# Performance work log

Measured on AMD Instinct MI355X. Metric: run time of the kernel, lower is better.

The kernel has to match this reference:

```python
import math
import jax, jax.numpy as jnp
import numpy as np

HIDDEN = 2880
HEAD_DIM = 64
N_HEADS = 64
N_KV = 8
Q_MULT = N_HEADS // N_KV  # 8
QKV_DIM = HEAD_DIM * (N_HEADS + 2 * N_KV)  # 5120
SLIDING_WINDOW = 128
SM_SCALE = 1.0 / math.sqrt(HEAD_DIM)
ROPE_BASE = 150000.0
ROPE_SCALING = 32.0
INIT_CTX = 4096
NTK_ALPHA = 1.0
NTK_BETA = 32.0
EPS = 1e-5
N_TOKENS = 1536


def rope_tables(n):
    # YaRN-style inv_freq mixing (scaling_factor > 1 branch)
    d = HEAD_DIM
    freq = ROPE_BASE ** (jnp.arange(0, d, 2, dtype=jnp.float32) / d)
    concentration = 0.1 * math.log(ROPE_SCALING) + 1.0
    d_half = d / 2
    low = d_half * math.log(INIT_CTX / (NTK_BETA * 2 * math.pi)) / math.log(ROPE_BASE)
    high = d_half * math.log(INIT_CTX / (NTK_ALPHA * 2 * math.pi)) / math.log(ROPE_BASE)
    interpolation = 1.0 / (ROPE_SCALING * freq)
    extrapolation = 1.0 / freq
    ramp = (jnp.arange(d_half, dtype=jnp.float32) - low) / (high - low)
    mask = 1.0 - jnp.clip(ramp, 0.0, 1.0)
    inv_freq = interpolation * (1.0 - mask) + extrapolation * mask
    t = jnp.arange(n, dtype=jnp.float32)
    freqs = t[:, None] * inv_freq[None, :]  # (n, d/2)
    return jnp.cos(freqs) * concentration, jnp.sin(freqs) * concentration


def apply_rotary(x, cos, sin):
    # x: (n, H, d); cos/sin: (n, d/2)
    c = cos[:, None, :]
    s = sin[:, None, :]
    x1, x2 = jnp.split(x, 2, axis=-1)
    return jnp.concatenate([x1 * c - x2 * s, x2 * c + x1 * s], axis=-1)


def setup_inputs() -> dict:
    key = jax.random.key(0)
    ks = jax.random.split(key, 7)
    x = jax.random.normal(ks[0], (N_TOKENS, HIDDEN), dtype=jnp.float32)
    norm_scale = jnp.ones((HIDDEN,), dtype=jnp.float32)
    qkv_w = jax.random.normal(ks[1], (QKV_DIM, HIDDEN), dtype=jnp.float32) * 0.02
    qkv_b = jax.random.normal(ks[2], (QKV_DIM,), dtype=jnp.float32) * 0.02
    out_w = jax.random.normal(ks[3], (HIDDEN, HEAD_DIM * N_HEADS), dtype=jnp.float32) * 0.02
    out_b = jax.random.normal(ks[4], (HIDDEN,), dtype=jnp.float32) * 0.02
    sinks = jax.random.normal(ks[5], (N_HEADS,), dtype=jnp.float32)
    return {"x": x, "norm_scale": norm_scale, "qkv_w": qkv_w, "qkv_b": qkv_b,
            "out_w": out_w, "out_b": out_b, "sinks": sinks}


def reference(x, norm_scale, qkv_w, qkv_b, out_w, out_b, sinks):
    n = x.shape[0]
    # RMSNorm (fp32)
    t = x * jax.lax.rsqrt(jnp.mean(x * x, axis=-1, keepdims=True) + EPS) * norm_scale
    # fused QKV projection
    qkv = t @ qkv_w.T + qkv_b  # (n, QKV_DIM)
    q = qkv[:, : N_HEADS * HEAD_DIM].reshape(n, N_KV, Q_MULT, HEAD_DIM)
    k = qkv[:, N_HEADS * HEAD_DIM : (N_HEADS + N_KV) * HEAD_DIM].reshape(n, N_KV, HEAD_DIM)
    v = qkv[:, (N_HEADS + N_KV) * HEAD_DIM :].reshape(n, N_KV, HEAD_DIM)
    # RoPE
    cos, sin = rope_tables(n)
    q = apply_rotary(q.reshape(n, N_HEADS, HEAD_DIM), cos, sin).reshape(n, N_KV, Q_MULT, HEAD_DIM)
    k = apply_rotary(k, cos, sin)
    # attention with causal + sliding-window mask and sink logits
    i = jnp.arange(n)[:, None]
    j = jnp.arange(n)[None, :]
    allowed = (j <= i) & (j > i - SLIDING_WINDOW)
    mask = jnp.where(allowed, 0.0, -jnp.inf).astype(jnp.float32)  # (q, k)
    scores = jnp.einsum('qhmd,khd->hmqk', q, k) * SM_SCALE + mask[None, None, :, :]
    s = sinks.reshape(N_KV, Q_MULT, 1, 1)
    s = jnp.broadcast_to(s, (N_KV, Q_MULT, n, 1))
    logits = jnp.concatenate([scores, s], axis=-1)
    w = jax.nn.softmax(logits, axis=-1)[..., :-1]  # drop sink column
    attn = jnp.einsum('hmqk,khd->qhmd', w, v).reshape(n, N_HEADS * HEAD_DIM)
    # output projection + residual
    return x + attn @ out_w.T + out_b
```

## Files before the change

### kernel.cpp

```cpp
#include <hip/hip_runtime.h>

typedef __attribute__((ext_vector_type(8))) short bf16x8;
typedef __attribute__((ext_vector_type(4))) float f32x4;

#define HIDDEN 2880
#define QKV_DIM 5120
#define NH 64
#define NKV 8
#define HD 64
#define ATT_DIM 4096
#define WINDOW 128
#define SM_SCALE 0.125f

__device__ __forceinline__ ushort f2bf(float f) {
  union { float f; unsigned u; } a; a.f = f;
  unsigned r = a.u + 0x7fffu + ((a.u >> 16) & 1u);
  return (ushort)(r >> 16);
}

__device__ __forceinline__ void gload_lds16(const void* g, void* l) {
  __builtin_amdgcn_global_load_lds((const __attribute__((address_space(1))) void*)g,
                                   (__attribute__((address_space(3))) void*)l, 16, 0, 0);
}

__global__ __launch_bounds__(256) void cvt_f32_bf16(const float* __restrict__ in,
                                                    ushort* __restrict__ out, int n4) {
  int i = blockIdx.x * blockDim.x + threadIdx.x;
  int stride = gridDim.x * blockDim.x;
  for (; i < n4; i += stride) {
    float4 v = ((const float4*)in)[i];
    ushort4 o = { f2bf(v.x), f2bf(v.y), f2bf(v.z), f2bf(v.w) };
    ((ushort4*)out)[i] = o;
  }
}

__global__ __launch_bounds__(256) void rmsnorm_bf16(const float* __restrict__ x,
                                                    const float* __restrict__ scale,
                                                    ushort* __restrict__ t) {
  int row = blockIdx.x;
  int tid = threadIdx.x;
  const float4* xr = (const float4*)(x + (size_t)row * HIDDEN);
  float4 a0 = xr[tid];
  float4 a1 = xr[tid + 256];
  bool has2 = tid < 208;
  float4 a2 = has2 ? xr[tid + 512] : float4{0.f, 0.f, 0.f, 0.f};
  float ss = a0.x*a0.x + a0.y*a0.y + a0.z*a0.z + a0.w*a0.w
           + a1.x*a1.x + a1.y*a1.y + a1.z*a1.z + a1.w*a1.w
           + a2.x*a2.x + a2.y*a2.y + a2.z*a2.z + a2.w*a2.w;
  for (int m = 1; m < 64; m <<= 1) ss += __shfl_xor(ss, m, 64);
  __shared__ float red[4];
  if ((tid & 63) == 0) red[tid >> 6] = ss;
  __syncthreads();
  ss = red[0] + red[1] + red[2] + red[3];
  float r = rsqrtf(ss / (float)HIDDEN + 1e-5f);
  ushort4* tr = (ushort4*)(t + (size_t)row * HIDDEN);
  const float4* sc4 = (const float4*)scale;
  {
    float4 s = sc4[tid];
    ushort4 o = { f2bf(a0.x*r*s.x), f2bf(a0.y*r*s.y), f2bf(a0.z*r*s.z), f2bf(a0.w*r*s.w) };
    tr[tid] = o;
  }
  {
    float4 s = sc4[tid + 256];
    ushort4 o = { f2bf(a1.x*r*s.x), f2bf(a1.y*r*s.y), f2bf(a1.z*r*s.z), f2bf(a1.w*r*s.w) };
    tr[tid + 256] = o;
  }
  if (has2) {
    float4 s = sc4[tid + 512];
    ushort4 o = { f2bf(a2.x*r*s.x), f2bf(a2.y*r*s.y), f2bf(a2.z*r*s.z), f2bf(a2.w*r*s.w) };
    tr[tid + 512] = o;
  }
}

template <int MASK_N>
__global__ __launch_bounds__(512)
void gemm_8p(const ushort* __restrict__ A, const ushort* __restrict__ B,
             float* __restrict__ P, int M, int N, int K, int NSK) {
  __shared__ __align__(16) ushort Al[2][256 * 64];
  __shared__ __align__(16) ushort Bl[2][256 * 64];
  const int tid = threadIdx.x;
  const int wave = tid >> 6, lane = tid & 63;
  const int l15 = lane & 15, hi = lane >> 4;

  int nwg = gridDim.x, orig = blockIdx.x;
  int q8 = nwg >> 3, r8 = nwg & 7, xcd = orig & 7, seq = orig >> 3;
  int swz = (xcd < r8 ? xcd * (q8 + 1) : r8 * (q8 + 1) + (xcd - r8) * q8) + seq;
  int nm = M >> 8;
  int bm = swz % nm, bn = swz / nm;
  const int row0 = bm * 256, col0 = bn * 256;
  const int sk = blockIdx.y;
  const int NTtot = K >> 6;
  const int tt0 = sk * NTtot / NSK, tt1 = (sk + 1) * NTtot / NSK;
  float* Pp = P + (size_t)sk * M * N;

  const int wrow = (wave >> 2) * 128;
  const int wcol = (wave & 3) * 64;
  const int srow = lane >> 3;
  const int schunk = (lane & 7) ^ srow;

  f32x4 acc[8][4] = {};

  auto stageA = [&](int t, int r) {
    int row = row0 + r * 64 + wave * 8 + srow;
    gload_lds16(A + (size_t)row * K + (t << 6) + schunk * 8,
                &Al[t & 1][(r * 64 + wave * 8) * 64]);
  };
  auto stageB = [&](int t, int r) {
    int brow = col0 + r * 64 + wave * 8 + srow;
    if (MASK_N) { if (brow > N - 1) brow = N - 1; }
    gload_lds16(B + (size_t)brow * K + (t << 6) + schunk * 8,
                &Bl[t & 1][(r * 64 + wave * 8) * 64]);
  };
  auto stageAll = [&](int t) {
#pragma unroll
    for (int r = 0; r < 4; ++r) { stageA(t, r); stageB(t, r); }
  };
  auto LDA = [&](bf16x8 (&dst)[4][2], int mh, const char* base) {
#pragma unroll
    for (int mt = 0; mt < 4; ++mt)
#pragma unroll
      for (int ks = 0; ks < 2; ++ks) {
        int rr = wrow + mh * 64 + mt * 16 + l15;
        int off = (rr * 128 + ks * 64 + hi * 16) ^ ((rr & 7) << 4);
        dst[mt][ks] = *(const bf16x8*)(base + off);
      }
  };
  auto LDB = [&](bf16x8 (&dst)[2][2], int nh, const char* base) {
#pragma unroll
    for (int nt = 0; nt < 2; ++nt)
#pragma unroll
      for (int ks = 0; ks < 2; ++ks) {
        int rr = wcol + nh * 32 + nt * 16 + l15;
        int off = (rr * 128 + ks * 64 + hi * 16) ^ ((rr & 7) << 4);
        dst[nt][ks] = *(const bf16x8*)(base + off);
      }
  };
  auto MMA = [&](bf16x8 (&a)[4][2], bf16x8 (&b)[2][2], int mh, int nh) {
    __builtin_amdgcn_s_setprio(1);
#pragma unroll
    for (int ks = 0; ks < 2; ++ks)
#pragma unroll
      for (int nt = 0; nt < 2; ++nt)
#pragma unroll
        for (int mt = 0; mt < 4; ++mt)
          acc[mh * 4 + mt][nh * 2 + nt] = __builtin_amdgcn_mfma_f32_16x16x32_bf16(
              a[mt][ks], b[nt][ks], acc[mh * 4 + mt][nh * 2 + nt], 0, 0, 0);
    __builtin_amdgcn_s_setprio(0);
  };

  stageAll(tt0);
  bool two = (tt1 - tt0 > 1);
  if (two) {
    stageAll(tt0 + 1);
    asm volatile("s_waitcnt vmcnt(8)" ::: "memory");
  } else {
    asm volatile("s_waitcnt vmcnt(0)" ::: "memory");
  }
  __builtin_amdgcn_s_barrier();

  for (int t = tt0; t < tt1; ++t) {
    const char* Ab = (const char*)&Al[t & 1][0];
    const char* Bb = (const char*)&Bl[t & 1][0];
    bool pre = (t + 2 < tt1);
    bf16x8 afr[4][2], bf0[2][2], bf1[2][2];
    LDA(afr, 0, Ab);
    LDB(bf0, 0, Bb);
    __builtin_amdgcn_s_barrier();
    MMA(afr, bf0, 0, 0);
    __builtin_amdgcn_s_barrier();
    LDB(bf1, 1, Bb);
    if (pre) { stageA(t + 2, 0); stageA(t + 2, 2); }
    __builtin_amdgcn_s_barrier();
    MMA(afr, bf1, 0, 1);
    __builtin_amdgcn_s_barrier();
    LDA(afr, 1, Ab);
    if (pre) { stageB(t + 2, 0); stageB(t + 2, 1); stageB(t + 2, 2); stageB(t + 2, 3); }
    __builtin_amdgcn_s_barrier();
    MMA(afr, bf1, 1, 1);
    __builtin_amdgcn_s_barrier();
    if (pre) { stageA(t + 2, 1); stageA(t + 2, 3); }
    __builtin_amdgcn_s_barrier();
    MMA(afr, bf0, 1, 0);
    if (pre) asm volatile("s_waitcnt vmcnt(8)" ::: "memory");
    else     asm volatile("s_waitcnt vmcnt(0)" ::: "memory");
    __builtin_amdgcn_s_barrier();
  }

#pragma unroll
  for (int mtg = 0; mtg < 8; ++mtg) {
#pragma unroll
    for (int nt = 0; nt < 4; ++nt) {
#pragma unroll
      for (int rr = 0; rr < 4; ++rr) {
        int row = row0 + wrow + mtg * 16 + (hi << 2) + rr;
        int col = col0 + wcol + nt * 16 + l15;
        if (!MASK_N || col < N) Pp[(size_t)row * N + col] = acc[mtg][nt][rr];
      }
    }
  }
}

__global__ __launch_bounds__(256)
void reduce_out(const float* __restrict__ x, const float* __restrict__ b,
                const float* __restrict__ p, int nsk, size_t stride,
                float* __restrict__ out, int n4, int N) {
  int i = blockIdx.x * blockDim.x + threadIdx.x;
  if (i >= n4) return;
  float4 v = ((const float4*)x)[i];
  int col = (i * 4) % N;
  float4 bb = *(const float4*)(b + col);
  v.x += bb.x; v.y += bb.y; v.z += bb.z; v.w += bb.w;
  for (int s = 0; s < nsk; ++s) {
    float4 pv = *(const float4*)(p + s * stride + (size_t)i * 4);
    v.x += pv.x; v.y += pv.y; v.z += pv.z; v.w += pv.w;
  }
  ((float4*)out)[i] = v;
}

__global__ __launch_bounds__(256)
void rope_split(const float* __restrict__ p, size_t stride, const float* __restrict__ qkvb,
                ushort* __restrict__ qb, ushort* __restrict__ kb, ushort* __restrict__ vb) {
  int tok = blockIdx.x;
  int tid = threadIdx.x;
  __shared__ float cs[32], sn[32];
  if (tid < 32) {
    float d = (float)tid;
    float freq = powf(150000.0f, d / 32.0f);
    float conc = 0.1f * logf(32.0f) + 1.0f;
    float lg = logf(150000.0f);
    float low = 32.0f * logf(4096.0f / (32.0f * 6.2831853f)) / lg;
    float high = 32.0f * logf(4096.0f / 6.2831853f) / lg;
    float ramp = (d - low) / (high - low);
    float cl = fminf(fmaxf(ramp, 0.0f), 1.0f);
    float mask = 1.0f - cl;
    float inv_freq = (1.0f - mask) / (32.0f * freq) + mask / freq;
    float fr = (float)tok * inv_freq;
    cs[tid] = cosf(fr) * conc;
    sn[tid] = sinf(fr) * conc;
  }
  __syncthreads();
  const float* r0 = p + (size_t)tok * QKV_DIM;
  const float* r1 = r0 + stride;
  auto ld = [&](int c) { return r0[c] + r1[c] + qkvb[c]; };
#pragma unroll
  for (int it = 0; it < 8; ++it) {
    int pp = tid + it * 256;
    int hd = pp >> 5, d = pp & 31;
    float x1 = ld(hd * 64 + d), x2 = ld(hd * 64 + d + 32);
    float c = cs[d], s = sn[d];
    size_t o = ((size_t)tok * NH + hd) * HD + d;
    qb[o] = f2bf(x1 * c - x2 * s);
    qb[o + 32] = f2bf(x2 * c + x1 * s);
  }
  {
    int pp = tid;
    int hd = pp >> 5, d = pp & 31;
    float x1 = ld(4096 + hd * 64 + d), x2 = ld(4096 + hd * 64 + d + 32);
    float c = cs[d], s = sn[d];
    size_t o = ((size_t)tok * NKV + hd) * HD + d;
    kb[o] = f2bf(x1 * c - x2 * s);
    kb[o + 32] = f2bf(x2 * c + x1 * s);
  }
#pragma unroll
  for (int it = 0; it < 2; ++it) {
    int pp = tid + it * 256;
    vb[(size_t)tok * (NKV * HD) + pp] = f2bf(ld(4608 + pp));
  }
}

__global__ __launch_bounds__(512)
void attn_fused(const ushort* __restrict__ qb, const ushort* __restrict__ kb,
                const ushort* __restrict__ vb, const float* __restrict__ sinks,
                ushort* __restrict__ attn, int n) {
  __shared__ __align__(16) ushort Kl[160 * 64];
  __shared__ __align__(16) ushort Vt[64 * 168];
  __shared__ __align__(16) ushort Pl[8][16 * 40];
  int tid = threadIdx.x;
  int wave = tid >> 6, lane = tid & 63;
  int l15 = lane & 15, hi = lane >> 4;
  int qstart = blockIdx.x * 16;
  int kv = blockIdx.y;
  int head = kv * 8 + wave;
  int key0 = qstart - 128;

  for (int i = 0; i < 3; ++i) {
    int rowb = i * 64 + wave * 8;
    if (rowb < 160) {
      int r = rowb + (lane >> 3);
      int gj = key0 + r; if (gj < 0) gj = 0;
      int chunk = (lane & 7) ^ (lane >> 3);
      gload_lds16(kb + ((size_t)gj * NKV + kv) * HD + chunk * 8, Kl + rowb * 64);
    }
  }
  for (int e = tid; e < 160 * 16; e += 512) {
    int j = e >> 4, d4 = (e & 15) << 2;
    int gj = key0 + j; if (gj < 0) gj = 0;
    ushort4 v = *(const ushort4*)(vb + ((size_t)gj * NKV + kv) * HD + d4);
    Vt[(d4 + 0) * 168 + j] = v.x;
    Vt[(d4 + 1) * 168 + j] = v.y;
    Vt[(d4 + 2) * 168 + j] = v.z;
    Vt[(d4 + 3) * 168 + j] = v.w;
  }
  bf16x8 qf[2];
#pragma unroll
  for (int ks = 0; ks < 2; ++ks) {
    int r = qstart + l15;
    int kk = ks * 32 + hi * 8;
    qf[ks] = *(const bf16x8*)(qb + ((size_t)r * NH + head) * HD + kk);
  }
  __syncthreads();

  f32x4 s[10] = {};
#pragma unroll
  for (int nt = 0; nt < 10; ++nt) {
#pragma unroll
    for (int ks = 0; ks < 2; ++ks) {
      int r = nt * 16 + l15;
      int off = (r * 128 + (ks * 32 + hi * 8) * 2) ^ ((r & 7) << 4);
      bf16x8 kf = *(const bf16x8*)((const char*)Kl + off);
      s[nt] = __builtin_amdgcn_mfma_f32_16x16x32_bf16(qf[ks], kf, s[nt], 0, 0, 0);
    }
  }

  float lrow[4];
  float snk = sinks[head];
#pragma unroll
  for (int r = 0; r < 4; ++r) {
    int i = qstart + hi * 4 + r;
    float mx = -1e30f;
#pragma unroll
    for (int nt = 0; nt < 10; ++nt) {
      int j = key0 + nt * 16 + l15;
      bool ok = (j >= 0) && (j <= i) && (j > i - WINDOW);
      float val = ok ? s[nt][r] * SM_SCALE : -1e30f;
      s[nt][r] = val;
      mx = fmaxf(mx, val);
    }
    mx = fmaxf(mx, __shfl_xor(mx, 1, 64));
    mx = fmaxf(mx, __shfl_xor(mx, 2, 64));
    mx = fmaxf(mx, __shfl_xor(mx, 4, 64));
    mx = fmaxf(mx, __shfl_xor(mx, 8, 64));
    mx = fmaxf(mx, snk);
    float sum = 0.f;
#pragma unroll
    for (int nt = 0; nt < 10; ++nt) {
      float pv = __expf(s[nt][r] - mx);
      s[nt][r] = pv;
      sum += pv;
    }
    sum += __shfl_xor(sum, 1, 64);
    sum += __shfl_xor(sum, 2, 64);
    sum += __shfl_xor(sum, 4, 64);
    sum += __shfl_xor(sum, 8, 64);
    sum += __expf(snk - mx);
    lrow[r] = sum;
  }

  f32x4 o[4] = {};
#pragma unroll
  for (int kc = 0; kc < 5; ++kc) {
#pragma unroll
    for (int t2 = 0; t2 < 2; ++t2) {
      int nt = kc * 2 + t2;
#pragma unroll
      for (int r = 0; r < 4; ++r)
        Pl[wave][(hi * 4 + r) * 40 + t2 * 16 + l15] = f2bf(s[nt][r]);
    }
    bf16x8 pa = *(const bf16x8*)(&Pl[wave][l15 * 40 + hi * 8]);
#pragma unroll
    for (int nt = 0; nt < 4; ++nt) {
      int d = nt * 16 + l15;
      int kk = kc * 32 + hi * 8;
      bf16x8 vf = *(const bf16x8*)(&Vt[d * 168 + kk]);
      o[nt] = __builtin_amdgcn_mfma_f32_16x16x32_bf16(pa, vf, o[nt], 0, 0, 0);
    }
  }

#pragma unroll
  for (int nt = 0; nt < 4; ++nt)
#pragma unroll
    for (int r = 0; r < 4; ++r) {
      int row = qstart + hi * 4 + r;
      int d = nt * 16 + l15;
      float val = o[nt][r] / lrow[r];
      attn[((size_t)row * NH + head) * HD + d] = f2bf(val);
    }
}

extern "C" void kernel_launch(void* const* d_in, const int* in_sizes, int n_in,
                              void* d_out, int out_size, void* d_ws, size_t ws_size,
                              hipStream_t stream) {
  const float* x      = (const float*)d_in[0];
  const float* nscale = (const float*)d_in[1];
  const float* qkv_w  = (const float*)d_in[2];
  const float* qkv_b  = (const float*)d_in[3];
  const float* out_w  = (const float*)d_in[4];
  const float* out_b  = (const float*)d_in[5];
  const float* sinks  = (const float*)d_in[6];
  float* out = (float*)d_out;
  int n = in_sizes[0] / HIDDEN;

  char* ws = (char*)d_ws;
  size_t off = 0;
  auto alloc = [&](size_t bytes) {
    char* p = ws + off;
    off += (bytes + 255) & ~(size_t)255;
    return p;
  };
  ushort* t_bf    = (ushort*)alloc((size_t)n * HIDDEN * 2);
  ushort* qkvw_bf = (ushort*)alloc((size_t)QKV_DIM * HIDDEN * 2);
  ushort* outw_bf = (ushort*)alloc((size_t)HIDDEN * ATT_DIM * 2);
  ushort* q_bf    = (ushort*)alloc((size_t)n * NH * HD * 2);
  ushort* k_bf    = (ushort*)alloc((size_t)n * NKV * HD * 2);
  ushort* v_bf    = (ushort*)alloc((size_t)n * NKV * HD * 2);
  ushort* attn    = (ushort*)alloc((size_t)n * ATT_DIM * 2);
  size_t qkv_ps = (size_t)n * QKV_DIM;
  size_t out_ps = (size_t)n * HIDDEN;
  size_t pelems = 2 * qkv_ps > 3 * out_ps ? 2 * qkv_ps : 3 * out_ps;
  float* partials = (float*)alloc(pelems * 4);

  cvt_f32_bf16<<<2048, 256, 0, stream>>>(qkv_w, qkvw_bf, QKV_DIM * HIDDEN / 4);
  cvt_f32_bf16<<<2048, 256, 0, stream>>>(out_w, outw_bf, HIDDEN * ATT_DIM / 4);
  rmsnorm_bf16<<<n, 256, 0, stream>>>(x, nscale, t_bf);
  gemm_8p<0><<<dim3((n / 256) * (QKV_DIM / 256), 2), 512, 0, stream>>>(
      t_bf, qkvw_bf, partials, n, QKV_DIM, HIDDEN, 2);
  rope_split<<<n, 256, 0, stream>>>(partials, qkv_ps, qkv_b, q_bf, k_bf, v_bf);
  attn_fused<<<dim3(n / 16, NKV), 512, 0, stream>>>(q_bf, k_bf, v_bf, sinks, attn, n);
  gemm_8p<1><<<dim3((n / 256) * 12, 3), 512, 0, stream>>>(
      attn, outw_bf, partials, n, HIDDEN, ATT_DIM, 3);
  reduce_out<<<(n * HIDDEN / 4 + 255) / 256, 256, 0, stream>>>(
      x, out_b, partials, 3, out_ps, out, n * HIDDEN / 4, HIDDEN);
}
```

Measured before the change: 180.6 us.

## Replace split-K 256x256 GEMMs with smaller-tile triple-buffered GEMMs and fused epilogue

Replaces the split-K 256x256 GEMM with a 128xBROWS tile GEMM that uses a three-stage LDS ring buffer and no split-K. The QKV GEMM now writes its result once and the RoPE kernel reads a single buffer. The output projection uses 128x192 tiles, which cover HIDDEN exactly and remove the N masking, and adds bias and residual in its epilogue, so the reduce kernel is gone. This drops the partial-sum writes and reads and one kernel launch. In exchange each block does a longer K loop with a smaller tile, which changes arithmetic intensity and occupancy.

```diff
diff --git a/kernel.cpp b/kernel.cpp
--- a/kernel.cpp
+++ b/kernel.cpp
@@ -72,12 +72,14 @@
   }
 }
 
-template <int MASK_N>
+template <int NFRAG, int EPI>
 __global__ __launch_bounds__(512)
-void gemm_8p(const ushort* __restrict__ A, const ushort* __restrict__ B,
-             float* __restrict__ P, int M, int N, int K, int NSK) {
-  __shared__ __align__(16) ushort Al[2][256 * 64];
-  __shared__ __align__(16) ushort Bl[2][256 * 64];
+void gemm_3b(const ushort* __restrict__ A, const ushort* __restrict__ B,
+             const float* __restrict__ bias, const float* __restrict__ resid,
+             float* __restrict__ C, int M, int N, int K) {
+  constexpr int BROWS = 64 * NFRAG;
+  __shared__ __align__(16) ushort Al[3][128 * 64];
+  __shared__ __align__(16) ushort Bl[3][BROWS * 64];
   const int tid = threadIdx.x;
   const int wave = tid >> 6, lane = tid & 63;
   const int l15 = lane & 15, hi = lane >> 4;
@@ -85,140 +87,108 @@
   int nwg = gridDim.x, orig = blockIdx.x;
   int q8 = nwg >> 3, r8 = nwg & 7, xcd = orig & 7, seq = orig >> 3;
   int swz = (xcd < r8 ? xcd * (q8 + 1) : r8 * (q8 + 1) + (xcd - r8) * q8) + seq;
-  int nm = M >> 8;
+  int nm = M >> 7;
   int bm = swz % nm, bn = swz / nm;
-  const int row0 = bm * 256, col0 = bn * 256;
-  const int sk = blockIdx.y;
-  const int NTtot = K >> 6;
-  const int tt0 = sk * NTtot / NSK, tt1 = (sk + 1) * NTtot / NSK;
-  float* Pp = P + (size_t)sk * M * N;
-
-  const int wrow = (wave >> 2) * 128;
-  const int wcol = (wave & 3) * 64;
+  const int row0 = bm * 128, col0 = bn * BROWS;
+  const int wrow = (wave >> 2) * 64;
+  const int wcol = (wave & 3) * (16 * NFRAG);
   const int srow = lane >> 3;
   const int schunk = (lane & 7) ^ srow;
-
-  f32x4 acc[8][4] = {};
-
-  auto stageA = [&](int t, int r) {
-    int row = row0 + r * 64 + wave * 8 + srow;
-    gload_lds16(A + (size_t)row * K + (t << 6) + schunk * 8,
-                &Al[t & 1][(r * 64 + wave * 8) * 64]);
-  };
-  auto stageB = [&](int t, int r) {
-    int brow = col0 + r * 64 + wave * 8 + srow;
-    if (MASK_N) { if (brow > N - 1) brow = N - 1; }
-    gload_lds16(B + (size_t)brow * K + (t << 6) + schunk * 8,
-                &Bl[t & 1][(r * 64 + wave * 8) * 64]);
-  };
-  auto stageAll = [&](int t) {
-#pragma unroll
-    for (int r = 0; r < 4; ++r) { stageA(t, r); stageB(t, r); }
-  };
-  auto LDA = [&](bf16x8 (&dst)[4][2], int mh, const char* base) {
-#pragma unroll
-    for (int mt = 0; mt < 4; ++mt)
-#pragma unroll
-      for (int ks = 0; ks < 2; ++ks) {
-        int rr = wrow + mh * 64 + mt * 16 + l15;
-        int off = (rr * 128 + ks * 64 + hi * 16) ^ ((rr & 7) << 4);
-        dst[mt][ks] = *(const bf16x8*)(base + off);
+  const int NT = K >> 6;
+
+  f32x4 acc[4][NFRAG] = {};
+
+  auto stageA = [&](int t) {
+    int b = t % 3, k0 = t << 6;
+#pragma unroll
+    for (int r = 0; r < 2; ++r) {
+      int rowb = wave * 16 + r * 8;
+      gload_lds16(A + (size_t)(row0 + rowb + srow) * K + k0 + schunk * 8, &Al[b][rowb * 64]);
+    }
+  };
+  auto stageB = [&](int t) {
+    int b = t % 3, k0 = t << 6;
+#pragma unroll
+    for (int r = 0; r < NFRAG; ++r) {
+      int rowb = wave * (8 * NFRAG) + r * 8;
+      gload_lds16(B + (size_t)(col0 + rowb + srow) * K + k0 + schunk * 8, &Bl[b][rowb * 64]);
+    }
+  };
+  auto LDA = [&](bf16x8 (&dst)[4], int ks, const char* base) {
+#pragma unroll
+    for (int mt = 0; mt < 4; ++mt) {
+      int rr = wrow + mt * 16 + l15;
+      int off = (rr * 128 + ks * 64 + hi * 16) ^ ((rr & 7) << 4);
+      dst[mt] = *(const bf16x8*)(base + off);
+    }
+  };
+  auto LDB = [&](bf16x8 (&dst)[NFRAG], int ks, const char* base) {
+#pragma unroll
+    for (int nt = 0; nt < NFRAG; ++nt) {
+      int rr = wcol + nt * 16 + l15;
+      int off = (rr * 128 + ks * 64 + hi * 16) ^ ((rr & 7) << 4);
+      dst[nt] = *(const bf16x8*)(base + off);
+    }
+  };
+  auto MMA = [&](bf16x8 (&a)[4], bf16x8 (&b)[NFRAG]) {
+    __builtin_amdgcn_s_setprio(1);
+#pragma unroll
+    for (int nt = 0; nt < NFRAG; ++nt)
+#pragma unroll
+      for (int mt = 0; mt < 4; ++mt)
+        acc[mt][nt] = __builtin_amdgcn_mfma_f32_16x16x32_bf16(a[mt], b[nt], acc[mt][nt], 0, 0, 0);
+    __builtin_amdgcn_s_setprio(0);
+  };
+
+  stageA(0); stageB(0);
+  stageA(1); stageB(1);
+  if constexpr (NFRAG == 4) asm volatile("s_waitcnt vmcnt(6)" ::: "memory");
+  else                      asm volatile("s_waitcnt vmcnt(5)" ::: "memory");
+  __builtin_amdgcn_s_barrier();
+
+  for (int t = 0; t < NT; ++t) {
+    const char* Ab = (const char*)&Al[t % 3][0];
+    const char* Bb = (const char*)&Bl[t % 3][0];
+    bool pre = (t + 2 < NT);
+    bf16x8 af[4], bf[NFRAG];
+    LDA(af, 0, Ab);
+    LDB(bf, 0, Bb);
+    if (pre) stageA(t + 2);
+    __builtin_amdgcn_s_barrier();
+    MMA(af, bf);
+    __builtin_amdgcn_s_barrier();
+    LDA(af, 1, Ab);
+    LDB(bf, 1, Bb);
+    if (pre) stageB(t + 2);
+    __builtin_amdgcn_s_barrier();
+    MMA(af, bf);
+    if (pre) {
+      if constexpr (NFRAG == 4) asm volatile("s_waitcnt vmcnt(6)" ::: "memory");
+      else                      asm volatile("s_waitcnt vmcnt(5)" ::: "memory");
+    } else {
+      asm volatile("s_waitcnt vmcnt(0)" ::: "memory");
+    }
+    __builtin_amdgcn_s_barrier();
+  }
+
+#pragma unroll
+  for (int mt = 0; mt < 4; ++mt) {
+#pragma unroll
+    for (int nt = 0; nt < NFRAG; ++nt) {
+#pragma unroll
+      for (int rr = 0; rr < 4; ++rr) {
+        int row = row0 + wrow + mt * 16 + (hi << 2) + rr;
+        int col = col0 + wcol + nt * 16 + l15;
+        float v = acc[mt][nt][rr];
+        if (EPI == 1) v += bias[col] + resid[(size_t)row * N + col];
+        C[(size_t)row * N + col] = v;
       }
-  };
-  auto LDB = [&](bf16x8 (&dst)[2][2], int nh, const char* base) {
-#pragma unroll
-    for (int nt = 0; nt < 2; ++nt)
-#pragma unroll
-      for (int ks = 0; ks < 2; ++ks) {
-        int rr = wcol + nh * 32 + nt * 16 + l15;
-        int off = (rr * 128 + ks * 64 + hi * 16) ^ ((rr & 7) << 4);
-        dst[nt][ks] = *(const bf16x8*)(base + off);
-      }
-  };
-  auto MMA = [&](bf16x8 (&a)[4][2], bf16x8 (&b)[2][2], int mh, int nh) {
-    __builtin_amdgcn_s_setprio(1);
-#pragma unroll
-    for (int ks = 0; ks < 2; ++ks)
-#pragma unroll
-      for (int nt = 0; nt < 2; ++nt)
-#pragma unroll
-        for (int mt = 0; mt < 4; ++mt)
-          acc[mh * 4 + mt][nh * 2 + nt] = __builtin_amdgcn_mfma_f32_16x16x32_bf16(
-              a[mt][ks], b[nt][ks], acc[mh * 4 + mt][nh * 2 + nt], 0, 0, 0);
-    __builtin_amdgcn_s_setprio(0);
-  };
-
-  stageAll(tt0);
-  bool two = (tt1 - tt0 > 1);
-  if (two) {
-    stageAll(tt0 + 1);
-    asm volatile("s_waitcnt vmcnt(8)" ::: "memory");
-  } else {
-    asm volatile("s_waitcnt vmcnt(0)" ::: "memory");
-  }
-  __builtin_amdgcn_s_barrier();
-
-  for (int t = tt0; t < tt1; ++t) {
-    const char* Ab = (const char*)&Al[t & 1][0];
-    const char* Bb = (const char*)&Bl[t & 1][0];
-    bool pre = (t + 2 < tt1);
-    bf16x8 afr[4][2], bf0[2][2], bf1[2][2];
-    LDA(afr, 0, Ab);
-    LDB(bf0, 0, Bb);
-    __builtin_amdgcn_s_barrier();
-    MMA(afr, bf0, 0, 0);
-    __builtin_amdgcn_s_barrier();
-    LDB(bf1, 1, Bb);
-    if (pre) { stageA(t + 2, 0); stageA(t + 2, 2); }
-    __builtin_amdgcn_s_barrier();
-    MMA(afr, bf1, 0, 1);
-    __builtin_amdgcn_s_barrier();
-    LDA(afr, 1, Ab);
-    if (pre) { stageB(t + 2, 0); stageB(t + 2, 1); stageB(t + 2, 2); stageB(t + 2, 3); }
-    __builtin_amdgcn_s_barrier();
-    MMA(afr, bf1, 1, 1);
-    __builtin_amdgcn_s_barrier();
-    if (pre) { stageA(t + 2, 1); stageA(t + 2, 3); }
-    __builtin_amdgcn_s_barrier();
-    MMA(afr, bf0, 1, 0);
-    if (pre) asm volatile("s_waitcnt vmcnt(8)" ::: "memory");
-    else     asm volatile("s_waitcnt vmcnt(0)" ::: "memory");
-    __builtin_amdgcn_s_barrier();
-  }
-
-#pragma unroll
-  for (int mtg = 0; mtg < 8; ++mtg) {
-#pragma unroll
-    for (int nt = 0; nt < 4; ++nt) {
-#pragma unroll
-      for (int rr = 0; rr < 4; ++rr) {
-        int row = row0 + wrow + mtg * 16 + (hi << 2) + rr;
-        int col = col0 + wcol + nt * 16 + l15;
-        if (!MASK_N || col < N) Pp[(size_t)row * N + col] = acc[mtg][nt][rr];
-      }
     }
   }
 }
 
 __global__ __launch_bounds__(256)
-void reduce_out(const float* __restrict__ x, const float* __restrict__ b,
-                const float* __restrict__ p, int nsk, size_t stride,
-                float* __restrict__ out, int n4, int N) {
-  int i = blockIdx.x * blockDim.x + threadIdx.x;
-  if (i >= n4) return;
-  float4 v = ((const float4*)x)[i];
-  int col = (i * 4) % N;
-  float4 bb = *(const float4*)(b + col);
-  v.x += bb.x; v.y += bb.y; v.z += bb.z; v.w += bb.w;
-  for (int s = 0; s < nsk; ++s) {
-    float4 pv = *(const float4*)(p + s * stride + (size_t)i * 4);
-    v.x += pv.x; v.y += pv.y; v.z += pv.z; v.w += pv.w;
-  }
-  ((float4*)out)[i] = v;
-}
-
-__global__ __launch_bounds__(256)
-void rope_split(const float* __restrict__ p, size_t stride, const float* __restrict__ qkvb,
+void rope_split(const float* __restrict__ qkv, const float* __restrict__ qkvb,
                 ushort* __restrict__ qb, ushort* __restrict__ kb, ushort* __restrict__ vb) {
   int tok = blockIdx.x;
   int tid = threadIdx.x;
@@ -239,9 +209,8 @@
     sn[tid] = sinf(fr) * conc;
   }
   __syncthreads();
-  const float* r0 = p + (size_t)tok * QKV_DIM;
-  const float* r1 = r0 + stride;
-  auto ld = [&](int c) { return r0[c] + r1[c] + qkvb[c]; };
+  const float* row = qkv + (size_t)tok * QKV_DIM;
+  auto ld = [&](int c) { return row[c] + qkvb[c]; };
 #pragma unroll
   for (int it = 0; it < 8; ++it) {
     int pp = tid + it * 256;
@@ -410,24 +379,19 @@
   ushort* t_bf    = (ushort*)alloc((size_t)n * HIDDEN * 2);
   ushort* qkvw_bf = (ushort*)alloc((size_t)QKV_DIM * HIDDEN * 2);
   ushort* outw_bf = (ushort*)alloc((size_t)HIDDEN * ATT_DIM * 2);
+  float*  qkv     = (float*)alloc((size_t)n * QKV_DIM * 4);
   ushort* q_bf    = (ushort*)alloc((size_t)n * NH * HD * 2);
   ushort* k_bf    = (ushort*)alloc((size_t)n * NKV * HD * 2);
   ushort* v_bf    = (ushort*)alloc((size_t)n * NKV * HD * 2);
   ushort* attn    = (ushort*)alloc((size_t)n * ATT_DIM * 2);
-  size_t qkv_ps = (size_t)n * QKV_DIM;
-  size_t out_ps = (size_t)n * HIDDEN;
-  size_t pelems = 2 * qkv_ps > 3 * out_ps ? 2 * qkv_ps : 3 * out_ps;
-  float* partials = (float*)alloc(pelems * 4);
 
   cvt_f32_bf16<<<2048, 256, 0, stream>>>(qkv_w, qkvw_bf, QKV_DIM * HIDDEN / 4);
   cvt_f32_bf16<<<2048, 256, 0, stream>>>(out_w, outw_bf, HIDDEN * ATT_DIM / 4);
   rmsnorm_bf16<<<n, 256, 0, stream>>>(x, nscale, t_bf);
-  gemm_8p<0><<<dim3((n / 256) * (QKV_DIM / 256), 2), 512, 0, stream>>>(
-      t_bf, qkvw_bf, partials, n, QKV_DIM, HIDDEN, 2);
-  rope_split<<<n, 256, 0, stream>>>(partials, qkv_ps, qkv_b, q_bf, k_bf, v_bf);
+  gemm_3b<4, 0><<<(n / 128) * (QKV_DIM / 256), 512, 0, stream>>>(
+      t_bf, qkvw_bf, nullptr, nullptr, qkv, n, QKV_DIM, HIDDEN);
+  rope_split<<<n, 256, 0, stream>>>(qkv, qkv_b, q_bf, k_bf, v_bf);
   attn_fused<<<dim3(n / 16, NKV), 512, 0, stream>>>(q_bf, k_bf, v_bf, sinks, attn, n);
-  gemm_8p<1><<<dim3((n / 256) * 12, 3), 512, 0, stream>>>(
-      attn, outw_bf, partials, n, HIDDEN, ATT_DIM, 3);
-  reduce_out<<<(n * HIDDEN / 4 + 255) / 256, 256, 0, stream>>>(
-      x, out_b, partials, 3, out_ps, out, n * HIDDEN / 4, HIDDEN);
-}
+  gemm_3b<3, 1><<<(n / 128) * (HIDDEN / 192), 512, 0, stream>>>(
+      attn, outw_bf, out_b, x, out, n, HIDDEN, ATT_DIM);
+}
```

Result: no change. 178.6 us (-1.1%).

## Fuse fp32-to-bf16 weight conversion into GEMM B-tile staging

Applied to the files above, without the earlier changes.

Removes the two standalone weight conversion kernels. The GEMMs now read fp32 weights directly into registers, pack them to bf16, and write them into the swizzled LDS tile. This avoids writing bf16 weight copies to memory and reading them back. In exchange, each weight tile is fetched at twice the byte width, possibly several times across M-tiles and split-K blocks, and the pipeline uses more registers and VALU work for the conversion and synchronous LDS writes.

```diff
diff --git a/kernel.cpp b/kernel.cpp
--- a/kernel.cpp
+++ b/kernel.cpp
@@ -18,20 +18,18 @@
   return (ushort)(r >> 16);
 }
 
+__device__ __forceinline__ bf16x8 pack_bf16x8(float4 a, float4 b) {
+  bf16x8 r;
+  r[0] = (short)f2bf(a.x); r[1] = (short)f2bf(a.y);
+  r[2] = (short)f2bf(a.z); r[3] = (short)f2bf(a.w);
+  r[4] = (short)f2bf(b.x); r[5] = (short)f2bf(b.y);
+  r[6] = (short)f2bf(b.z); r[7] = (short)f2bf(b.w);
+  return r;
+}
+
 __device__ __forceinline__ void gload_lds16(const void* g, void* l) {
   __builtin_amdgcn_global_load_lds((const __attribute__((address_space(1))) void*)g,
                                    (__attribute__((address_space(3))) void*)l, 16, 0, 0);
-}
-
-__global__ __launch_bounds__(256) void cvt_f32_bf16(const float* __restrict__ in,
-                                                    ushort* __restrict__ out, int n4) {
-  int i = blockIdx.x * blockDim.x + threadIdx.x;
-  int stride = gridDim.x * blockDim.x;
-  for (; i < n4; i += stride) {
-    float4 v = ((const float4*)in)[i];
-    ushort4 o = { f2bf(v.x), f2bf(v.y), f2bf(v.z), f2bf(v.w) };
-    ((ushort4*)out)[i] = o;
-  }
 }
 
 __global__ __launch_bounds__(256) void rmsnorm_bf16(const float* __restrict__ x,
@@ -74,7 +72,7 @@
 
 template <int MASK_N>
 __global__ __launch_bounds__(512)
-void gemm_8p(const ushort* __restrict__ A, const ushort* __restrict__ B,
+void gemm_8p(const ushort* __restrict__ A, const float* __restrict__ Bf,
              float* __restrict__ P, int M, int N, int K, int NSK) {
   __shared__ __align__(16) ushort Al[2][256 * 64];
   __shared__ __align__(16) ushort Bl[2][256 * 64];
@@ -97,6 +95,7 @@
   const int wcol = (wave & 3) * 64;
   const int srow = lane >> 3;
   const int schunk = (lane & 7) ^ srow;
+  const int gchunk8 = ((lane & 7) ^ srow) * 8;
 
   f32x4 acc[8][4] = {};
 
@@ -105,15 +104,24 @@
     gload_lds16(A + (size_t)row * K + (t << 6) + schunk * 8,
                 &Al[t & 1][(r * 64 + wave * 8) * 64]);
   };
-  auto stageB = [&](int t, int r) {
-    int brow = col0 + r * 64 + wave * 8 + srow;
-    if (MASK_N) { if (brow > N - 1) brow = N - 1; }
-    gload_lds16(B + (size_t)brow * K + (t << 6) + schunk * 8,
-                &Bl[t & 1][(r * 64 + wave * 8) * 64]);
-  };
-  auto stageAll = [&](int t) {
-#pragma unroll
-    for (int r = 0; r < 4; ++r) { stageA(t, r); stageB(t, r); }
+  auto loadB = [&](float4 (&breg)[4][2], int t) {
+#pragma unroll
+    for (int g = 0; g < 4; ++g) {
+      int rit = wave * 32 + g * 8 + srow;
+      int brow = col0 + rit;
+      if (MASK_N) { if (brow > N - 1) brow = N - 1; }
+      const float4* src = (const float4*)(Bf + (size_t)brow * K + (t << 6) + gchunk8);
+      breg[g][0] = src[0];
+      breg[g][1] = src[1];
+    }
+  };
+  auto writeB = [&](float4 (&breg)[4][2], int t) {
+#pragma unroll
+    for (int g = 0; g < 4; ++g) {
+      int rit = wave * 32 + g * 8 + srow;
+      *(bf16x8*)((char*)&Bl[t & 1][0] + rit * 128 + (lane & 7) * 16) =
+          pack_bf16x8(breg[g][0], breg[g][1]);
+    }
   };
   auto LDA = [&](bf16x8 (&dst)[4][2], int mh, const char* base) {
 #pragma unroll
@@ -148,13 +156,20 @@
     __builtin_amdgcn_s_setprio(0);
   };
 
-  stageAll(tt0);
-  bool two = (tt1 - tt0 > 1);
-  if (two) {
-    stageAll(tt0 + 1);
-    asm volatile("s_waitcnt vmcnt(8)" ::: "memory");
-  } else {
-    asm volatile("s_waitcnt vmcnt(0)" ::: "memory");
+  {
+    float4 br[4][2];
+#pragma unroll
+    for (int r = 0; r < 4; ++r) stageA(tt0, r);
+    loadB(br, tt0); writeB(br, tt0);
+    bool two = (tt1 - tt0 > 1);
+    if (two) {
+#pragma unroll
+      for (int r = 0; r < 4; ++r) stageA(tt0 + 1, r);
+      loadB(br, tt0 + 1); writeB(br, tt0 + 1);
+      asm volatile("s_waitcnt vmcnt(4) lgkmcnt(0)" ::: "memory");
+    } else {
+      asm volatile("s_waitcnt vmcnt(0) lgkmcnt(0)" ::: "memory");
+    }
   }
   __builtin_amdgcn_s_barrier();
 
@@ -163,8 +178,10 @@
     const char* Bb = (const char*)&Bl[t & 1][0];
     bool pre = (t + 2 < tt1);
     bf16x8 afr[4][2], bf0[2][2], bf1[2][2];
+    float4 breg[4][2];
     LDA(afr, 0, Ab);
     LDB(bf0, 0, Bb);
+    if (pre) loadB(breg, t + 2);
     __builtin_amdgcn_s_barrier();
     MMA(afr, bf0, 0, 0);
     __builtin_amdgcn_s_barrier();
@@ -174,14 +191,15 @@
     MMA(afr, bf1, 0, 1);
     __builtin_amdgcn_s_barrier();
     LDA(afr, 1, Ab);
-    if (pre) { stageB(t + 2, 0); stageB(t + 2, 1); stageB(t + 2, 2); stageB(t + 2, 3); }
+    if (pre) writeB(breg, t + 2);
     __builtin_amdgcn_s_barrier();
     MMA(afr, bf1, 1, 1);
+    asm volatile("s_waitcnt lgkmcnt(0)" ::: "memory");
     __builtin_amdgcn_s_barrier();
     if (pre) { stageA(t + 2, 1); stageA(t + 2, 3); }
     __builtin_amdgcn_s_barrier();
     MMA(afr, bf0, 1, 0);
-    if (pre) asm volatile("s_waitcnt vmcnt(8)" ::: "memory");
+    if (pre) asm volatile("s_waitcnt vmcnt(4)" ::: "memory");
     else     asm volatile("s_waitcnt vmcnt(0)" ::: "memory");
     __builtin_amdgcn_s_barrier();
   }
@@ -408,8 +426,6 @@
     return p;
   };
   ushort* t_bf    = (ushort*)alloc((size_t)n * HIDDEN * 2);
-  ushort* qkvw_bf = (ushort*)alloc((size_t)QKV_DIM * HIDDEN * 2);
-  ushort* outw_bf = (ushort*)alloc((size_t)HIDDEN * ATT_DIM * 2);
   ushort* q_bf    = (ushort*)alloc((size_t)n * NH * HD * 2);
   ushort* k_bf    = (ushort*)alloc((size_t)n * NKV * HD * 2);
   ushort* v_bf    = (ushort*)alloc((size_t)n * NKV * HD * 2);
@@ -419,15 +435,13 @@
   size_t pelems = 2 * qkv_ps > 3 * out_ps ? 2 * qkv_ps : 3 * out_ps;
   float* partials = (float*)alloc(pelems * 4);
 
-  cvt_f32_bf16<<<2048, 256, 0, stream>>>(qkv_w, qkvw_bf, QKV_DIM * HIDDEN / 4);
-  cvt_f32_bf16<<<2048, 256, 0, stream>>>(out_w, outw_bf, HIDDEN * ATT_DIM / 4);
   rmsnorm_bf16<<<n, 256, 0, stream>>>(x, nscale, t_bf);
   gemm_8p<0><<<dim3((n / 256) * (QKV_DIM / 256), 2), 512, 0, stream>>>(
-      t_bf, qkvw_bf, partials, n, QKV_DIM, HIDDEN, 2);
+      t_bf, qkv_w, partials, n, QKV_DIM, HIDDEN, 2);
   rope_split<<<n, 256, 0, stream>>>(partials, qkv_ps, qkv_b, q_bf, k_bf, v_bf);
   attn_fused<<<dim3(n / 16, NKV), 512, 0, stream>>>(q_bf, k_bf, v_bf, sinks, attn, n);
   gemm_8p<1><<<dim3((n / 256) * 12, 3), 512, 0, stream>>>(
-      attn, outw_bf, partials, n, HIDDEN, ATT_DIM, 3);
+      attn, out_w, partials, n, HIDDEN, ATT_DIM, 3);
   reduce_out<<<(n * HIDDEN / 4 + 255) / 256, 256, 0, stream>>>(
       x, out_b, partials, 3, out_ps, out, n * HIDDEN / 4, HIDDEN);
 }
```

New measurement: 391.1 us. +116.5%, slower.

## Store split-K partials in bf16 and fuse out_w conversion into attention launch

Applied to the files above, without the earlier changes.

The split-K GEMM partial sums are now written as bf16 rather than fp32, which halves the write and read traffic between the GEMMs and the rope/reduce kernels. The out_w fp32-to-bf16 conversion moves into extra blocks appended to the attention grid, so it runs alongside attention instead of as a separate serial launch. The qkv_w conversion grid is also shrunk. Rounding each partial to bf16 before summing adds precision loss in the QKV activations and the final output, which risks tolerance failures.

```diff
diff --git a/kernel.cpp b/kernel.cpp
--- a/kernel.cpp
+++ b/kernel.cpp
@@ -16,6 +16,10 @@
   union { float f; unsigned u; } a; a.f = f;
   unsigned r = a.u + 0x7fffu + ((a.u >> 16) & 1u);
   return (ushort)(r >> 16);
+}
+__device__ __forceinline__ float bf2f(ushort u) {
+  union { unsigned u; float f; } a; a.u = ((unsigned)u) << 16;
+  return a.f;
 }
 
 __device__ __forceinline__ void gload_lds16(const void* g, void* l) {
@@ -75,7 +79,7 @@
 template <int MASK_N>
 __global__ __launch_bounds__(512)
 void gemm_8p(const ushort* __restrict__ A, const ushort* __restrict__ B,
-             float* __restrict__ P, int M, int N, int K, int NSK) {
+             ushort* __restrict__ P, int M, int N, int K, int NSK) {
   __shared__ __align__(16) ushort Al[2][256 * 64];
   __shared__ __align__(16) ushort Bl[2][256 * 64];
   const int tid = threadIdx.x;
@@ -91,7 +95,7 @@
   const int sk = blockIdx.y;
   const int NTtot = K >> 6;
   const int tt0 = sk * NTtot / NSK, tt1 = (sk + 1) * NTtot / NSK;
-  float* Pp = P + (size_t)sk * M * N;
+  ushort* Pp = P + (size_t)sk * M * N;
 
   const int wrow = (wave >> 2) * 128;
   const int wcol = (wave & 3) * 64;
@@ -194,7 +198,7 @@
       for (int rr = 0; rr < 4; ++rr) {
         int row = row0 + wrow + mtg * 16 + (hi << 2) + rr;
         int col = col0 + wcol + nt * 16 + l15;
-        if (!MASK_N || col < N) Pp[(size_t)row * N + col] = acc[mtg][nt][rr];
+        if (!MASK_N || col < N) Pp[(size_t)row * N + col] = f2bf(acc[mtg][nt][rr]);
       }
     }
   }
@@ -202,7 +206,7 @@
 
 __global__ __launch_bounds__(256)
 void reduce_out(const float* __restrict__ x, const float* __restrict__ b,
-                const float* __restrict__ p, int nsk, size_t stride,
+                const ushort* __restrict__ p, int nsk, size_t stride,
                 float* __restrict__ out, int n4, int N) {
   int i = blockIdx.x * blockDim.x + threadIdx.x;
   if (i >= n4) return;
@@ -211,14 +215,14 @@
   float4 bb = *(const float4*)(b + col);
   v.x += bb.x; v.y += bb.y; v.z += bb.z; v.w += bb.w;
   for (int s = 0; s < nsk; ++s) {
-    float4 pv = *(const float4*)(p + s * stride + (size_t)i * 4);
-    v.x += pv.x; v.y += pv.y; v.z += pv.z; v.w += pv.w;
+    ushort4 pv = *(const ushort4*)(p + s * stride + (size_t)i * 4);
+    v.x += bf2f(pv.x); v.y += bf2f(pv.y); v.z += bf2f(pv.z); v.w += bf2f(pv.w);
   }
   ((float4*)out)[i] = v;
 }
 
 __global__ __launch_bounds__(256)
-void rope_split(const float* __restrict__ p, size_t stride, const float* __restrict__ qkvb,
+void rope_split(const ushort* __restrict__ p, size_t stride, const float* __restrict__ qkvb,
                 ushort* __restrict__ qb, ushort* __restrict__ kb, ushort* __restrict__ vb) {
   int tok = blockIdx.x;
   int tid = threadIdx.x;
@@ -239,9 +243,9 @@
     sn[tid] = sinf(fr) * conc;
   }
   __syncthreads();
-  const float* r0 = p + (size_t)tok * QKV_DIM;
-  const float* r1 = r0 + stride;
-  auto ld = [&](int c) { return r0[c] + r1[c] + qkvb[c]; };
+  const ushort* r0 = p + (size_t)tok * QKV_DIM;
+  const ushort* r1 = r0 + stride;
+  auto ld = [&](int c) { return bf2f(r0[c]) + bf2f(r1[c]) + qkvb[c]; };
 #pragma unroll
   for (int it = 0; it < 8; ++it) {
     int pp = tid + it * 256;
@@ -269,17 +273,28 @@
 }
 
 __global__ __launch_bounds__(512)
-void attn_fused(const ushort* __restrict__ qb, const ushort* __restrict__ kb,
-                const ushort* __restrict__ vb, const float* __restrict__ sinks,
-                ushort* __restrict__ attn, int n) {
+void attn_cvt(const ushort* __restrict__ qb, const ushort* __restrict__ kb,
+              const ushort* __restrict__ vb, const float* __restrict__ sinks,
+              ushort* __restrict__ attn, int n, int nattn,
+              const float* __restrict__ w, ushort* __restrict__ wout, int n4w) {
   __shared__ __align__(16) ushort Kl[160 * 64];
   __shared__ __align__(16) ushort Vt[64 * 168];
   __shared__ __align__(16) ushort Pl[8][16 * 40];
   int tid = threadIdx.x;
+  if ((int)blockIdx.x >= nattn) {
+    int i = ((int)blockIdx.x - nattn) * 512 + tid;
+    int stride = (gridDim.x - nattn) * 512;
+    for (; i < n4w; i += stride) {
+      float4 v = ((const float4*)w)[i];
+      ushort4 o = { f2bf(v.x), f2bf(v.y), f2bf(v.z), f2bf(v.w) };
+      ((ushort4*)wout)[i] = o;
+    }
+    return;
+  }
   int wave = tid >> 6, lane = tid & 63;
   int l15 = lane & 15, hi = lane >> 4;
-  int qstart = blockIdx.x * 16;
-  int kv = blockIdx.y;
+  int qstart = ((int)blockIdx.x >> 3) * 16;
+  int kv = (int)blockIdx.x & 7;
   int head = kv * 8 + wave;
   int key0 = qstart - 128;
 
@@ -417,15 +432,16 @@
   size_t qkv_ps = (size_t)n * QKV_DIM;
   size_t out_ps = (size_t)n * HIDDEN;
   size_t pelems = 2 * qkv_ps > 3 * out_ps ? 2 * qkv_ps : 3 * out_ps;
-  float* partials = (float*)alloc(pelems * 4);
-
-  cvt_f32_bf16<<<2048, 256, 0, stream>>>(qkv_w, qkvw_bf, QKV_DIM * HIDDEN / 4);
-  cvt_f32_bf16<<<2048, 256, 0, stream>>>(out_w, outw_bf, HIDDEN * ATT_DIM / 4);
+  ushort* partials = (ushort*)alloc(pelems * 2);
+
+  cvt_f32_bf16<<<1024, 256, 0, stream>>>(qkv_w, qkvw_bf, QKV_DIM * HIDDEN / 4);
   rmsnorm_bf16<<<n, 256, 0, stream>>>(x, nscale, t_bf);
   gemm_8p<0><<<dim3((n / 256) * (QKV_DIM / 256), 2), 512, 0, stream>>>(
       t_bf, qkvw_bf, partials, n, QKV_DIM, HIDDEN, 2);
   rope_split<<<n, 256, 0, stream>>>(partials, qkv_ps, qkv_b, q_bf, k_bf, v_bf);
-  attn_fused<<<dim3(n / 16, NKV), 512, 0, stream>>>(q_bf, k_bf, v_bf, sinks, attn, n);
+  int nattn = (n / 16) * NKV;
+  attn_cvt<<<nattn + 320, 512, 0, stream>>>(q_bf, k_bf, v_bf, sinks, attn, n, nattn,
+                                            out_w, outw_bf, HIDDEN * ATT_DIM / 4);
   gemm_8p<1><<<dim3((n / 256) * 12, 3), 512, 0, stream>>>(
       attn, outw_bf, partials, n, HIDDEN, ATT_DIM, 3);
   reduce_out<<<(n * HIDDEN / 4 + 255) / 256, 256, 0, stream>>>(
```

Result: faster. 168.6 us (-6.7%).
